# Kernel optimization log

Measured on AMD Instinct MI355X. Metric: run time of the kernel, lower is better.

## Reference

```python
import jax, jax.numpy as jnp
import numpy as np

# Token / dim constants (from vm_step.Token and vm_step._SetDim)
CODE_START, CODE_END, MEM = 256, 257, 258
ADDR_KEY, MEM_STORE = 206, 455
VOCAB, D_MODEL = 272, 512
B, S = 16, 8192


def setup_inputs() -> dict:
    key = jax.random.key(0)
    k1, k2 = jax.random.split(key)
    token_ids = jax.random.randint(k1, (B, S), 0, VOCAB)
    embed_weight = jax.random.normal(k2, (VOCAB, D_MODEL), dtype=jnp.float32) * 0.02
    return {"token_ids": token_ids, "embed_weight": embed_weight, "mem_history_end": 2048}


def _augment_mask(token_ids, mem_history_end):
    """Boolean [B, S, D_MODEL] mask of positions that get set to 1.0."""
    Bb, Ss = token_ids.shape
    idx = jnp.arange(Ss)                                  # [S]
    is_start = token_ids == CODE_START
    is_end = token_ids == CODE_END
    # loop breaks at the FIRST CODE_END in each row
    end_idx = jnp.min(jnp.where(is_end, idx[None, :], Ss), axis=1)      # [B]
    # cs_pos = index of most recent CODE_START at-or-before i (-1 if none)
    cs = jax.lax.cummax(jnp.where(is_start, idx[None, :], -1), axis=1)  # [B,S]
    addr = idx[None, :] - cs - 1                                        # [B,S]
    valid = (cs >= 0) & (idx[None, :] < end_idx[:, None]) \
            & (token_ids < 256) & (addr >= 0)
    lo = addr & 15
    hi = (addr >> 4) & 15
    top = (addr >> 8) & 15
    bins = jnp.arange(16)                                 # nibble one-hots
    lo_oh = (bins == lo[..., None]) & valid[..., None]    # [B,S,16]
    hi_oh = (bins == hi[..., None]) & valid[..., None]
    top_oh = (bins == top[..., None]) & valid[..., None]
    mem_flag = (token_ids == MEM) & (idx[None, :] < mem_history_end)    # [B,S]

    mask = jnp.zeros((Bb, Ss, D_MODEL), dtype=bool)
    mask = mask.at[:, :, ADDR_KEY:ADDR_KEY + 16].set(lo_oh)
    mask = mask.at[:, :, ADDR_KEY + 16:ADDR_KEY + 32].set(hi_oh)
    mask = mask.at[:, :, ADDR_KEY + 32:ADDR_KEY + 48].set(top_oh)
    mask = mask.at[:, :, MEM_STORE].set(mem_flag)
    return mask


def reference(token_ids, embed_weight, mem_history_end):
    x = embed_weight[token_ids]                           # [B,S,D] gather
    mask = _augment_mask(token_ids, mem_history_end)
    return jnp.where(mask, jnp.asarray(1.0, x.dtype), x)
```

## Files before the change

### kernel.cpp

```cpp
#include <hip/hip_runtime.h>

#define TOK_CODE_START 256
#define TOK_CODE_END   257
#define TOK_MEM        258
#define ADDR_KEY       206
#define MEM_STORE      455

constexpr int Bb = 16;
constexpr int Ss = 8192;
constexpr int DM = 512;
constexpr int POS_PER_BLK = 64;
constexpr int QPP = DM / 4;
constexpr int THREADS = 256;

typedef float f32x4 __attribute__((ext_vector_type(4)));

__global__ __launch_bounds__(THREADS) void vm_fused_kernel(
    const int* __restrict__ tok,
    const f32x4* __restrict__ emb,
    const int* __restrict__ mhe_p,
    f32x4* __restrict__ out)
{
    const int bk = blockIdx.x;
    const int b  = bk >> 7;
    const int c  = bk & 127;
    const int t  = threadIdx.x;
    const int lane = t & 63;
    const int wid  = t >> 6;
    const int s0 = c * POS_PER_BLK;
    const int* row = tok + b * Ss;
    const int mhe = mhe_p[0];

    __shared__ int sP[4], sE[4];
    __shared__ unsigned int smask[POS_PER_BLK];

    int myTok = 0;
    if (t < POS_PER_BLK) myTok = row[s0 + t];

    int maxStart = -1;
    int minEnd = Ss;
    {
        const int base = t * 32;
        if (base < s0) {
            #pragma unroll
            for (int j = 0; j < 8; ++j) {
                int4 v = reinterpret_cast<const int4*>(row + base + j * 4)[0];
                int i0 = base + j * 4;
                if (v.x == TOK_CODE_START) maxStart = i0;
                if (v.y == TOK_CODE_START) maxStart = i0 + 1;
                if (v.z == TOK_CODE_START) maxStart = i0 + 2;
                if (v.w == TOK_CODE_START) maxStart = i0 + 3;
                if (v.x == TOK_CODE_END && minEnd == Ss) minEnd = i0;
                if (v.y == TOK_CODE_END && minEnd == Ss) minEnd = i0 + 1;
                if (v.z == TOK_CODE_END && minEnd == Ss) minEnd = i0 + 2;
                if (v.w == TOK_CODE_END && minEnd == Ss) minEnd = i0 + 3;
            }
        }
    }
    #pragma unroll
    for (int off = 32; off > 0; off >>= 1) {
        int u = __shfl_xor(maxStart, off);
        if (u > maxStart) maxStart = u;
        int w = __shfl_xor(minEnd, off);
        if (w < minEnd) minEnd = w;
    }
    if (lane == 0) { sP[wid] = maxStart; sE[wid] = minEnd; }
    __syncthreads();

    if (t < POS_PER_BLK) {
        int P = max(max(sP[0], sP[1]), max(sP[2], sP[3]));
        int E = min(min(sE[0], sE[1]), min(sE[2], sE[3]));

        const int idx = s0 + t;
        int st = (myTok == TOK_CODE_START) ? idx : -1;
        int en = (myTok == TOK_CODE_END) ? idx : Ss;
        #pragma unroll
        for (int off = 1; off < 64; off <<= 1) {
            int u = __shfl_up(st, off);
            int v = __shfl_up(en, off);
            if (lane >= off) {
                if (u > st) st = u;
                if (v < en) en = v;
            }
        }
        int cs = max(P, st);
        int firstEnd = min(E, en);
        int addr = idx - cs - 1;
        bool valid = (cs >= 0) && (firstEnd > idx) && (myTok < 256) && (addr >= 0);
        bool memf  = (myTok == TOK_MEM) && (idx < mhe);
        unsigned int w = (unsigned int)myTok;
        if (valid) w |= (1u << 9) | ((unsigned int)addr << 11);
        if (memf)  w |= (1u << 10);
        smask[t] = w;
    }
    __syncthreads();

    const int outBase = bk * (POS_PER_BLK * QPP);
    #pragma unroll 8
    for (int i = 0; i < 32; ++i) {
        int q = i * THREADS + t;
        int pos = q >> 7;
        int dq = q & 127;
        unsigned int pw = smask[pos];
        int tk = (int)(pw & 511u);
        f32x4 v = emb[tk * QPP + dq];
        unsigned int flags = pw >> 9;
        if (flags) {
            bool valid = (flags & 1u) != 0u;
            bool memf  = (flags & 2u) != 0u;
            int addr = (int)(flags >> 2);
            int p0 = ADDR_KEY      + (addr & 15);
            int p1 = ADDR_KEY + 16 + ((addr >> 4) & 15);
            int p2 = ADDR_KEY + 32 + ((addr >> 8) & 15);
            int d0 = dq << 2;
            #pragma unroll
            for (int j = 0; j < 4; ++j) {
                int d = d0 + j;
                if ((valid && (d == p0 || d == p1 || d == p2)) ||
                    (memf && d == MEM_STORE)) v[j] = 1.0f;
            }
        }
        __builtin_nontemporal_store(v, &out[outBase + q]);
    }
}

extern "C" void kernel_launch(void* const* d_in, const int* in_sizes, int n_in,
                              void* d_out, int out_size, void* d_ws, size_t ws_size,
                              hipStream_t stream) {
    const int* tok = (const int*)d_in[0];
    const f32x4* emb = (const f32x4*)d_in[1];
    const int* mhe = (const int*)d_in[2];
    f32x4* out = (f32x4*)d_out;

    vm_fused_kernel<<<Bb * (Ss / POS_PER_BLK), THREADS, 0, stream>>>(tok, emb, mhe, out);
}
```

Baseline: 58.21 us.

## Split prefix scan into separate summary kernel and drop nontemporal stores

Adds a small per-row kernel that computes each 64-position chunk's exclusive prefix of last CODE_START and first CODE_END and writes it to workspace. The gather kernel reads that summary instead of rescanning all earlier tokens of the row in every block, which removes quadratic redundant token reads. It also replaces nontemporal stores with ordinary stores. The cost is a second launch with a serial dependency and a tiny kernel that uses only 16 blocks.

```diff
diff --git a/kernel.cpp b/kernel.cpp
--- a/kernel.cpp
+++ b/kernel.cpp
@@ -9,15 +9,58 @@
 constexpr int Bb = 16;
 constexpr int Ss = 8192;
 constexpr int DM = 512;
-constexpr int POS_PER_BLK = 64;
+constexpr int CHUNK = 64;
+constexpr int NCH = Ss / CHUNK;
 constexpr int QPP = DM / 4;
-constexpr int THREADS = 256;
 
 typedef float f32x4 __attribute__((ext_vector_type(4)));
 
-__global__ __launch_bounds__(THREADS) void vm_fused_kernel(
+__global__ __launch_bounds__(128) void vm_summary_kernel(
+    const int* __restrict__ tok,
+    int2* __restrict__ summ)
+{
+    const int b = blockIdx.x;
+    const int t = threadIdx.x;
+    const int lane = t & 63;
+    const int w = t >> 6;
+    const int* chunk = tok + b * Ss + t * CHUNK;
+
+    int maxStart = -1, minEnd = Ss;
+    #pragma unroll
+    for (int j = 0; j < 16; ++j) {
+        int4 v = reinterpret_cast<const int4*>(chunk)[j];
+        int i0 = t * CHUNK + j * 4;
+        if (v.x == TOK_CODE_START) maxStart = i0;
+        if (v.y == TOK_CODE_START) maxStart = i0 + 1;
+        if (v.z == TOK_CODE_START) maxStart = i0 + 2;
+        if (v.w == TOK_CODE_START) maxStart = i0 + 3;
+        if (v.x == TOK_CODE_END && minEnd == Ss) minEnd = i0;
+        if (v.y == TOK_CODE_END && minEnd == Ss) minEnd = i0 + 1;
+        if (v.z == TOK_CODE_END && minEnd == Ss) minEnd = i0 + 2;
+        if (v.w == TOK_CODE_END && minEnd == Ss) minEnd = i0 + 3;
+    }
+
+    int ms = maxStart, me = minEnd;
+    #pragma unroll
+    for (int off = 1; off < 64; off <<= 1) {
+        int u = __shfl_up(ms, off);
+        int v = __shfl_up(me, off);
+        if (lane >= off) { if (u > ms) ms = u; if (v < me) me = v; }
+    }
+    __shared__ int cMs, cMe;
+    if (w == 0 && lane == 63) { cMs = ms; cMe = me; }
+    __syncthreads();
+    int pms = __shfl_up(ms, 1);
+    int pme = __shfl_up(me, 1);
+    if (lane == 0) { pms = -1; pme = Ss; }
+    if (w == 1) { if (cMs > pms) pms = cMs; if (cMe < pme) pme = cMe; }
+    summ[b * NCH + t] = make_int2(pms, pme);
+}
+
+__global__ __launch_bounds__(256) void vm_gather_kernel(
     const int* __restrict__ tok,
     const f32x4* __restrict__ emb,
+    const int2* __restrict__ summ,
     const int* __restrict__ mhe_p,
     f32x4* __restrict__ out)
 {
@@ -26,79 +69,38 @@
     const int c  = bk & 127;
     const int t  = threadIdx.x;
     const int lane = t & 63;
-    const int wid  = t >> 6;
-    const int s0 = c * POS_PER_BLK;
-    const int* row = tok + b * Ss;
-    const int mhe = mhe_p[0];
+    const int s0 = c * CHUNK;
 
-    __shared__ int sP[4], sE[4];
-    __shared__ unsigned int smask[POS_PER_BLK];
+    __shared__ unsigned int smask[CHUNK];
 
-    int myTok = 0;
-    if (t < POS_PER_BLK) myTok = row[s0 + t];
-
-    int maxStart = -1;
-    int minEnd = Ss;
-    {
-        const int base = t * 32;
-        if (base < s0) {
-            #pragma unroll
-            for (int j = 0; j < 8; ++j) {
-                int4 v = reinterpret_cast<const int4*>(row + base + j * 4)[0];
-                int i0 = base + j * 4;
-                if (v.x == TOK_CODE_START) maxStart = i0;
-                if (v.y == TOK_CODE_START) maxStart = i0 + 1;
-                if (v.z == TOK_CODE_START) maxStart = i0 + 2;
-                if (v.w == TOK_CODE_START) maxStart = i0 + 3;
-                if (v.x == TOK_CODE_END && minEnd == Ss) minEnd = i0;
-                if (v.y == TOK_CODE_END && minEnd == Ss) minEnd = i0 + 1;
-                if (v.z == TOK_CODE_END && minEnd == Ss) minEnd = i0 + 2;
-                if (v.w == TOK_CODE_END && minEnd == Ss) minEnd = i0 + 3;
-            }
-        }
-    }
-    #pragma unroll
-    for (int off = 32; off > 0; off >>= 1) {
-        int u = __shfl_xor(maxStart, off);
-        if (u > maxStart) maxStart = u;
-        int w = __shfl_xor(minEnd, off);
-        if (w < minEnd) minEnd = w;
-    }
-    if (lane == 0) { sP[wid] = maxStart; sE[wid] = minEnd; }
-    __syncthreads();
-
-    if (t < POS_PER_BLK) {
-        int P = max(max(sP[0], sP[1]), max(sP[2], sP[3]));
-        int E = min(min(sE[0], sE[1]), min(sE[2], sE[3]));
-
-        const int idx = s0 + t;
-        int st = (myTok == TOK_CODE_START) ? idx : -1;
-        int en = (myTok == TOK_CODE_END) ? idx : Ss;
+    if (t < 64) {
+        const int idx = s0 + lane;
+        int tv = tok[b * Ss + idx];
+        int2 pe = summ[bk];
+        int st = (tv == TOK_CODE_START) ? idx : -1;
+        int en = (tv == TOK_CODE_END) ? idx : Ss;
         #pragma unroll
         for (int off = 1; off < 64; off <<= 1) {
             int u = __shfl_up(st, off);
             int v = __shfl_up(en, off);
-            if (lane >= off) {
-                if (u > st) st = u;
-                if (v < en) en = v;
-            }
+            if (lane >= off) { if (u > st) st = u; if (v < en) en = v; }
         }
-        int cs = max(P, st);
-        int firstEnd = min(E, en);
+        int cs = max(pe.x, st);
+        int fe = min(pe.y, en);
         int addr = idx - cs - 1;
-        bool valid = (cs >= 0) && (firstEnd > idx) && (myTok < 256) && (addr >= 0);
-        bool memf  = (myTok == TOK_MEM) && (idx < mhe);
-        unsigned int w = (unsigned int)myTok;
-        if (valid) w |= (1u << 9) | ((unsigned int)addr << 11);
-        if (memf)  w |= (1u << 10);
-        smask[t] = w;
+        bool valid = (cs >= 0) && (fe > idx) && (tv < 256) && (addr >= 0);
+        bool memf  = (tv == TOK_MEM) && (idx < mhe_p[0]);
+        unsigned int wd = (unsigned int)tv;
+        if (valid) wd |= (1u << 9) | ((unsigned int)addr << 11);
+        if (memf)  wd |= (1u << 10);
+        smask[lane] = wd;
     }
     __syncthreads();
 
-    const int outBase = bk * (POS_PER_BLK * QPP);
+    const int outBase = bk * (CHUNK * QPP);
     #pragma unroll 8
     for (int i = 0; i < 32; ++i) {
-        int q = i * THREADS + t;
+        int q = i * 256 + t;
         int pos = q >> 7;
         int dq = q & 127;
         unsigned int pw = smask[pos];
@@ -120,7 +122,7 @@
                     (memf && d == MEM_STORE)) v[j] = 1.0f;
             }
         }
-        __builtin_nontemporal_store(v, &out[outBase + q]);
+        out[outBase + q] = v;
     }
 }
 
@@ -130,7 +132,9 @@
     const int* tok = (const int*)d_in[0];
     const f32x4* emb = (const f32x4*)d_in[1];
     const int* mhe = (const int*)d_in[2];
+    int2* summ = (int2*)d_ws;
     f32x4* out = (f32x4*)d_out;
 
-    vm_fused_kernel<<<Bb * (Ss / POS_PER_BLK), THREADS, 0, stream>>>(tok, emb, mhe, out);
+    vm_summary_kernel<<<Bb, 128, 0, stream>>>(tok, summ);
+    vm_gather_kernel<<<Bb * NCH, 256, 0, stream>>>(tok, emb, summ, mhe, out);
 }
```

Result: faster. 53.61 us (-7.9%).
